# Optimization experiments

Hardware: AMD Instinct MI355X
Metric: run time of the kernel (lower is better)

The kernel has to match this reference:

```python
import jax, jax.numpy as jnp
import numpy as np

B, S, D, H = 8, 1024, 512, 8
DK = D // H
NEG = -1e30  # stands in for -inf; masked probs are zero-filled afterwards, so math matches


def setup_inputs() -> dict:
    rng = jax.random.key(0)
    ks = jax.random.split(rng, 12)
    f = lambda k, shape: jax.random.normal(k, shape, dtype=jnp.float32)
    w = lambda k: f(k, (D, D)) * 0.02  # stored as (in, out); y = x @ W + b
    return {
        "query": f(ks[0], (B, S, D)),
        "key": f(ks[1], (B, S, D)),
        "value": f(ks[2], (B, S, D)),
        "mask": jax.random.randint(ks[3], (B, 1, S), 0, 2, dtype=jnp.int32),
        "Wq": w(ks[4]), "bq": jnp.zeros((D,), jnp.float32),
        "Wk": w(ks[5]), "bk": jnp.zeros((D,), jnp.float32),
        "Wv": w(ks[6]), "bv": jnp.zeros((D,), jnp.float32),
        "Wo": w(ks[7]), "bo": jnp.zeros((D,), jnp.float32),
    }


def reference(query, key, value, mask, Wq, bq, Wk, bk, Wv, bv, Wo, bo):
    # QKV projections -> (B, H, S, DK)
    def proj(x, W, b):
        return (x @ W + b).reshape(B, -1, H, DK).transpose(0, 2, 1, 3)

    q = proj(query, Wq, bq)
    k = proj(key, Wk, bk)
    v = proj(value, Wv, bv)

    scores = jnp.einsum("bhqd,bhkd->bhqk", q, k) / jnp.sqrt(jnp.float32(DK))
    m = (mask[:, None, :, :] == 0)  # (B, 1, 1, S): True where masked out
    scores = jnp.where(m, NEG, scores)
    attn = jax.nn.softmax(scores, axis=-1)
    attn = jnp.where(m, 0.0, attn)  # dropout rate is 0.0 -> identity

    x = jnp.einsum("bhqk,bhkd->bhqd", attn, v)
    x = x.transpose(0, 2, 1, 3).reshape(B, -1, D)  # (B, S, D)
    return x @ Wo + bo
```

## Files before the change

### kernel.cpp

```cpp
#include <hip/hip_runtime.h>
#include <hip/hip_bf16.h>

#define NB 8
#define NS 1024
#define ND 512
#define NH 8
#define NDK 64

typedef __attribute__((ext_vector_type(8))) short bf16x8;
typedef __attribute__((ext_vector_type(4))) float f32x4;
typedef __attribute__((ext_vector_type(16))) float f32x16;

#define QSCALE 0.18033688011112042f
#define NEGBIG -3.0e38f

#define CVTPK(dst, a, b) \
    asm("v_cvt_pk_bf16_f32 %0, %1, %2" : "=v"(dst) : "v"(a), "v"(b))
#define PLSWAP(a, b) \
    asm("v_permlane32_swap_b32 %0, %1" : "+v"(a), "+v"(b))
#define GLOAD16(gp, lp)                                                        \
    __builtin_amdgcn_global_load_lds(                                          \
        (const __attribute__((address_space(1))) unsigned*)(gp),               \
        (__attribute__((address_space(3))) unsigned*)(lp), 16, 0, 0)

__device__ __forceinline__ unsigned short bfround(float f) {
    union { float f; unsigned u; } v; v.f = f;
    unsigned u = v.u;
    u += 0x7fffu + ((u >> 16) & 1u);
    return (unsigned short)(u >> 16);
}

__device__ __forceinline__ size_t qf_off(int s, int dk) {
    return ((size_t)(((s >> 5) * 4 + (dk >> 4)) * 64 + ((dk >> 3) & 1) * 32 + (s & 31)) << 3) + (dk & 7);
}
__device__ __forceinline__ size_t kf_off(int s, int dk) {
    return ((size_t)(((s >> 6) * 8 + ((s >> 5) & 1) * 4 + (dk >> 4)) * 64 + ((dk >> 3) & 1) * 32 + (s & 31)) << 3) + (dk & 7);
}
__device__ __forceinline__ size_t vf_off(int s, int dk) {
    return ((size_t)(((s >> 6) * 8 + (dk >> 5) * 4 + ((s >> 4) & 3)) * 64 + ((s >> 3) & 1) * 32 + (dk & 31)) << 3) + (s & 7);
}

__global__ __launch_bounds__(256) void wt_kernel(const float* __restrict__ W0,
                                                 const float* __restrict__ W1,
                                                 const float* __restrict__ W2,
                                                 const float* __restrict__ W3,
                                                 unsigned short* __restrict__ wt) {
    __shared__ float sh[64][65];
    const int z = blockIdx.z;
    const float* W = z == 0 ? W0 : z == 1 ? W1 : z == 2 ? W2 : W3;
    unsigned short* out = wt + (size_t)z * ND * ND;
    const int o0 = blockIdx.x * 64, i0 = blockIdx.y * 64;
    const int tx = threadIdx.x & 63;
    const int ty = threadIdx.x >> 6;
    #pragma unroll
    for (int rr = 0; rr < 16; ++rr) {
        const int row = ty * 16 + rr;
        sh[row][tx] = W[(size_t)(i0 + row) * ND + o0 + tx];
    }
    __syncthreads();
    #pragma unroll
    for (int rr = 0; rr < 16; ++rr) {
        const int row = ty * 16 + rr;
        out[(size_t)(o0 + row) * ND + i0 + tx] = bfround(sh[tx][row]);
    }
}

__global__ __launch_bounds__(256) void gemm_qkv(
    const float* __restrict__ A0, const float* __restrict__ A1, const float* __restrict__ A2,
    const unsigned short* __restrict__ wt,
    const float* __restrict__ b0, const float* __restrict__ b1, const float* __restrict__ b2,
    unsigned short* __restrict__ outb) {
    __shared__ float Asf[128 * 32];
    __shared__ unsigned short Bs[128 * 32];
    const int t = threadIdx.x;
    const int lane = t & 63, w = t >> 6;
    const int wr = w >> 1, wc = w & 1;
    const int lr = lane & 15, lg = lane >> 4;
    const int bid = blockIdx.x;
    const int u = (bid & 7) * 96 + (bid >> 3);
    const int xt = u & 3, yt = (u >> 2) & 63, z = u >> 8;
    const float* A = z == 0 ? A0 : z == 1 ? A1 : A2;
    const float* bias = z == 0 ? b0 : z == 1 ? b1 : b2;
    const unsigned short* Wt = wt + (size_t)z * ND * ND;
    unsigned short* outp = outb + (size_t)z * NB * NH * NS * NDK;
    const int m0 = yt * 128, n0 = xt * 128;

    const int a_row = w * 32 + (lane >> 3);
    const int a_gc = ((lane & 7) ^ (lane >> 3)) << 2;
    const int b_row = w * 32 + (lane >> 2);
    const int b_gc = (lane & 3) * 8;

    f32x4 acc[4][4];
    #pragma unroll
    for (int i = 0; i < 4; ++i)
        #pragma unroll
        for (int j = 0; j < 4; ++j) acc[i][j] = (f32x4){0.f, 0.f, 0.f, 0.f};

    for (int kt = 0; kt < 16; ++kt) {
        const int k0 = kt * 32;
        __syncthreads();
        #pragma unroll
        for (int j = 0; j < 4; ++j)
            GLOAD16(A + (size_t)(m0 + a_row + j * 8) * ND + k0 + a_gc,
                    Asf + (w * 4 + j) * 256);
        #pragma unroll
        for (int j = 0; j < 2; ++j)
            GLOAD16(Wt + (size_t)(n0 + b_row + j * 16) * ND + k0 + b_gc,
                    Bs + (w * 2 + j) * 512);
        __syncthreads();

        bf16x8 af[4], bfr[4];
        #pragma unroll
        for (int mi = 0; mi < 4; ++mi) {
            const int r = wr * 64 + mi * 16 + lr;
            const int u0 = (2 * lg) ^ (lr & 7), u1 = (2 * lg + 1) ^ (lr & 7);
            const f32x4 x0 = *(const f32x4*)(Asf + r * 32 + u0 * 4);
            const f32x4 x1 = *(const f32x4*)(Asf + r * 32 + u1 * 4);
            unsigned p0, p1, p2, p3;
            CVTPK(p0, x0[0], x0[1]); CVTPK(p1, x0[2], x0[3]);
            CVTPK(p2, x1[0], x1[1]); CVTPK(p3, x1[2], x1[3]);
            union { unsigned uu[4]; bf16x8 v; } c;
            c.uu[0] = p0; c.uu[1] = p1; c.uu[2] = p2; c.uu[3] = p3;
            af[mi] = c.v;
        }
        #pragma unroll
        for (int nj = 0; nj < 4; ++nj)
            bfr[nj] = *(const bf16x8*)(Bs + (wc * 64 + nj * 16 + lr) * 32 + lg * 8);
        #pragma unroll
        for (int mi = 0; mi < 4; ++mi)
            #pragma unroll
            for (int nj = 0; nj < 4; ++nj)
                acc[mi][nj] = __builtin_amdgcn_mfma_f32_16x16x32_bf16(
                    af[mi], bfr[nj], acc[mi][nj], 0, 0, 0);
    }

    const float osc = z == 0 ? QSCALE : 1.0f;
    #pragma unroll
    for (int mi = 0; mi < 4; ++mi) {
        #pragma unroll
        for (int nj = 0; nj < 4; ++nj) {
            const int n = n0 + wc * 64 + nj * 16 + lr;
            const float bv = bias[n];
            #pragma unroll
            for (int r = 0; r < 4; ++r) {
                const int m = m0 + wr * 64 + mi * 16 + lg * 4 + r;
                const float val = (acc[mi][nj][r] + bv) * osc;
                const int bb = m >> 10, s = m & 1023;
                const int hh = n >> 6, dk = n & 63;
                const size_t off = z == 0 ? qf_off(s, dk)
                                 : z == 1 ? kf_off(s, dk)
                                          : vf_off(s, dk);
                outp[((size_t)(bb * NH + hh) << 16) + off] = bfround(val);
            }
        }
    }
}

__global__ __launch_bounds__(256) void gemm_out(
    const unsigned short* __restrict__ Xb, const unsigned short* __restrict__ Wt,
    const float* __restrict__ bo, float* __restrict__ outp) {
    __shared__ unsigned short As[128 * 32];
    __shared__ unsigned short Bs[64 * 32];
    const int t = threadIdx.x;
    const int lane = t & 63, w = t >> 6;
    const int wr = w >> 1, wc = w & 1;
    const int lr = lane & 15, lg = lane >> 4;
    const int bid = blockIdx.x;
    const int u = (bid & 7) * 64 + (bid >> 3);
    const int xt = u & 7, yt = u >> 3;
    const int m0 = yt * 128, n0 = xt * 64;

    const int a_row = w * 32 + (lane >> 2);
    const int b_row = w * 16 + (lane >> 2);
    const int gc = (lane & 3) * 8;

    f32x4 acc[4][2];
    #pragma unroll
    for (int i = 0; i < 4; ++i)
        #pragma unroll
        for (int j = 0; j < 2; ++j) acc[i][j] = (f32x4){0.f, 0.f, 0.f, 0.f};

    for (int kt = 0; kt < 16; ++kt) {
        const int k0 = kt * 32;
        __syncthreads();
        #pragma unroll
        for (int j = 0; j < 2; ++j)
            GLOAD16(Xb + (size_t)(m0 + a_row + j * 16) * ND + k0 + gc,
                    As + (w * 2 + j) * 512);
        GLOAD16(Wt + (size_t)(n0 + b_row) * ND + k0 + gc, Bs + w * 512);
        __syncthreads();

        bf16x8 af[4], bfr[2];
        #pragma unroll
        for (int mi = 0; mi < 4; ++mi)
            af[mi] = *(const bf16x8*)(As + (wr * 64 + mi * 16 + lr) * 32 + lg * 8);
        #pragma unroll
        for (int nj = 0; nj < 2; ++nj)
            bfr[nj] = *(const bf16x8*)(Bs + (wc * 32 + nj * 16 + lr) * 32 + lg * 8);
        #pragma unroll
        for (int mi = 0; mi < 4; ++mi)
            #pragma unroll
            for (int nj = 0; nj < 2; ++nj)
                acc[mi][nj] = __builtin_amdgcn_mfma_f32_16x16x32_bf16(
                    af[mi], bfr[nj], acc[mi][nj], 0, 0, 0);
    }

    #pragma unroll
    for (int mi = 0; mi < 4; ++mi) {
        #pragma unroll
        for (int nj = 0; nj < 2; ++nj) {
            const int n = n0 + wc * 32 + nj * 16 + lr;
            const float bv = bo[n];
            #pragma unroll
            for (int r = 0; r < 4; ++r) {
                const int m = m0 + wr * 64 + mi * 16 + lg * 4 + r;
                outp[(size_t)m * ND + n] = acc[mi][nj][r] + bv;
            }
        }
    }
}

struct AttnState {
    f32x16 acc0, acc1;
    float m_st, l_st;
};

__device__ __forceinline__ void attn_step(const bf16x8 (&kf)[8], const bf16x8 (&vv)[8],
                                          const bf16x8 (&qf)[4], int mval,
                                          float* __restrict__ brow, int lane, int hi,
                                          AttnState& st) {
    brow[lane] = mval ? 0.f : NEGBIG;

    f32x16 sc0 = {}, sc1 = {};
    __builtin_amdgcn_s_setprio(1);
    sc0 = __builtin_amdgcn_mfma_f32_32x32x16_bf16(kf[0], qf[0], sc0, 0, 0, 0);
    sc1 = __builtin_amdgcn_mfma_f32_32x32x16_bf16(kf[4], qf[0], sc1, 0, 0, 0);
    sc0 = __builtin_amdgcn_mfma_f32_32x32x16_bf16(kf[1], qf[1], sc0, 0, 0, 0);
    sc1 = __builtin_amdgcn_mfma_f32_32x32x16_bf16(kf[5], qf[1], sc1, 0, 0, 0);
    sc0 = __builtin_amdgcn_mfma_f32_32x32x16_bf16(kf[2], qf[2], sc0, 0, 0, 0);
    sc1 = __builtin_amdgcn_mfma_f32_32x32x16_bf16(kf[6], qf[2], sc1, 0, 0, 0);
    sc0 = __builtin_amdgcn_mfma_f32_32x32x16_bf16(kf[3], qf[3], sc0, 0, 0, 0);
    sc1 = __builtin_amdgcn_mfma_f32_32x32x16_bf16(kf[7], qf[3], sc1, 0, 0, 0);
    __builtin_amdgcn_s_setprio(0);

    {
        const float* bl = brow + 4 * hi;
        #pragma unroll
        for (int mm = 0; mm < 4; ++mm) {
            const f32x4 bv0 = *(const f32x4*)(bl + 8 * mm);
            const f32x4 bv1 = *(const f32x4*)(bl + 32 + 8 * mm);
            #pragma unroll
            for (int c = 0; c < 4; ++c) {
                sc0[4 * mm + c] += bv0[c];
                sc1[4 * mm + c] += bv1[c];
            }
        }
    }

    float tv[16];
    #pragma unroll
    for (int r = 0; r < 16; ++r) tv[r] = fmaxf(sc0[r], sc1[r]);
    #pragma unroll
    for (int s = 8; s > 0; s >>= 1)
        #pragma unroll
        for (int r = 0; r < 16; ++r)
            if (r < s) tv[r] = fmaxf(tv[r], tv[r + s]);
    const float mx = fmaxf(tv[0], __shfl_xor(tv[0], 32));
    const float mn = fmaxf(st.m_st, mx);

    #pragma unroll
    for (int r = 0; r < 16; ++r) {
        sc0[r] = __builtin_amdgcn_exp2f(sc0[r] - mn);
        sc1[r] = __builtin_amdgcn_exp2f(sc1[r] - mn);
    }
    #pragma unroll
    for (int r = 0; r < 16; ++r) tv[r] = sc0[r] + sc1[r];
    #pragma unroll
    for (int s = 8; s > 0; s >>= 1)
        #pragma unroll
        for (int r = 0; r < 16; ++r)
            if (r < s) tv[r] += tv[r + s];
    const float rs = tv[0] + __shfl_xor(tv[0], 32);

    const bool ch = mn > st.m_st;
    if (__any(ch)) {
        const float f = __builtin_amdgcn_exp2f(st.m_st - mn);
        st.l_st = st.l_st * f + rs;
        st.m_st = mn;
        #pragma unroll
        for (int r = 0; r < 16; ++r) { st.acc0[r] *= f; st.acc1[r] *= f; }
    } else {
        st.l_st += rs;
    }

    union U8 { unsigned u[4]; bf16x8 v; };
    bf16x8 pA0, pA1, pB0, pB1;
    {
        unsigned w00, w01, w10, w11, w20, w21, w30, w31;
        CVTPK(w00, sc0[0], sc0[1]);  CVTPK(w01, sc0[2], sc0[3]);
        CVTPK(w10, sc0[4], sc0[5]);  CVTPK(w11, sc0[6], sc0[7]);
        CVTPK(w20, sc0[8], sc0[9]);  CVTPK(w21, sc0[10], sc0[11]);
        CVTPK(w30, sc0[12], sc0[13]); CVTPK(w31, sc0[14], sc0[15]);
        PLSWAP(w00, w10); PLSWAP(w01, w11);
        PLSWAP(w20, w30); PLSWAP(w21, w31);
        U8 f0; f0.u[0] = w00; f0.u[1] = w01; f0.u[2] = w10; f0.u[3] = w11;
        U8 f1; f1.u[0] = w20; f1.u[1] = w21; f1.u[2] = w30; f1.u[3] = w31;
        pA0 = f0.v; pA1 = f1.v;
    }
    {
        unsigned w00, w01, w10, w11, w20, w21, w30, w31;
        CVTPK(w00, sc1[0], sc1[1]);  CVTPK(w01, sc1[2], sc1[3]);
        CVTPK(w10, sc1[4], sc1[5]);  CVTPK(w11, sc1[6], sc1[7]);
        CVTPK(w20, sc1[8], sc1[9]);  CVTPK(w21, sc1[10], sc1[11]);
        CVTPK(w30, sc1[12], sc1[13]); CVTPK(w31, sc1[14], sc1[15]);
        PLSWAP(w00, w10); PLSWAP(w01, w11);
        PLSWAP(w20, w30); PLSWAP(w21, w31);
        U8 f0; f0.u[0] = w00; f0.u[1] = w01; f0.u[2] = w10; f0.u[3] = w11;
        U8 f1; f1.u[0] = w20; f1.u[1] = w21; f1.u[2] = w30; f1.u[3] = w31;
        pB0 = f0.v; pB1 = f1.v;
    }

    __builtin_amdgcn_s_setprio(1);
    st.acc0 = __builtin_amdgcn_mfma_f32_32x32x16_bf16(vv[0], pA0, st.acc0, 0, 0, 0);
    st.acc1 = __builtin_amdgcn_mfma_f32_32x32x16_bf16(vv[4], pA0, st.acc1, 0, 0, 0);
    st.acc0 = __builtin_amdgcn_mfma_f32_32x32x16_bf16(vv[1], pA1, st.acc0, 0, 0, 0);
    st.acc1 = __builtin_amdgcn_mfma_f32_32x32x16_bf16(vv[5], pA1, st.acc1, 0, 0, 0);
    st.acc0 = __builtin_amdgcn_mfma_f32_32x32x16_bf16(vv[2], pB0, st.acc0, 0, 0, 0);
    st.acc1 = __builtin_amdgcn_mfma_f32_32x32x16_bf16(vv[6], pB0, st.acc1, 0, 0, 0);
    st.acc0 = __builtin_amdgcn_mfma_f32_32x32x16_bf16(vv[3], pB1, st.acc0, 0, 0, 0);
    st.acc1 = __builtin_amdgcn_mfma_f32_32x32x16_bf16(vv[7], pB1, st.acc1, 0, 0, 0);
    __builtin_amdgcn_s_setprio(0);
}

__global__ __launch_bounds__(256, 2) void attn_kernel(const unsigned short* __restrict__ QF,
                                                      const unsigned short* __restrict__ KF,
                                                      const unsigned short* __restrict__ VF,
                                                      const int* __restrict__ mask,
                                                      unsigned short* __restrict__ Xb) {
    __shared__ float bias_lds[4][64];
    const int t = threadIdx.x;
    const int lane = t & 63, w = t >> 6;
    const int q32 = lane & 31, hi = lane >> 5;
    const int bid = blockIdx.x;
    const int u = (bid & 7) * 64 + (bid >> 3);
    const int bh = u >> 3, xq = u & 7;
    const int b = bh >> 3, h = bh & 7;
    const int q = xq * 128 + w * 32 + q32;
    const unsigned short* QFh = QF + ((size_t)bh << 16);
    const unsigned short* KFh = KF + ((size_t)bh << 16);
    const unsigned short* VFh = VF + ((size_t)bh << 16);
    const int* mk = mask + b * NS;
    float* brow = &bias_lds[w][0];

    bf16x8 qf[4];
    {
        const unsigned short* Qp = QFh + (size_t)(xq * 16 + w * 4) * 512 + lane * 8;
        qf[0] = *(const bf16x8*)(Qp + 0 * 512);
        qf[1] = *(const bf16x8*)(Qp + 1 * 512);
        qf[2] = *(const bf16x8*)(Qp + 2 * 512);
        qf[3] = *(const bf16x8*)(Qp + 3 * 512);
    }

    AttnState st;
    st.acc0 = (f32x16){}; st.acc1 = (f32x16){};
    st.m_st = -1.0e30f; st.l_st = 0.f;

    bf16x8 kA[8], kB[8], vv[8];

#define LOADK(dst, itx) do {                                                   \
        const unsigned short* _p = KFh + (size_t)(itx) * 4096 + lane * 8;      \
        dst[0] = *(const bf16x8*)(_p + 0 * 512);                               \
        dst[1] = *(const bf16x8*)(_p + 1 * 512);                               \
        dst[2] = *(const bf16x8*)(_p + 2 * 512);                               \
        dst[3] = *(const bf16x8*)(_p + 3 * 512);                               \
        dst[4] = *(const bf16x8*)(_p + 4 * 512);                               \
        dst[5] = *(const bf16x8*)(_p + 5 * 512);                               \
        dst[6] = *(const bf16x8*)(_p + 6 * 512);                               \
        dst[7] = *(const bf16x8*)(_p + 7 * 512);                               \
    } while (0)

#define LOADV(dst, itx) do {                                                   \
        const unsigned short* _p = VFh + (size_t)(itx) * 4096 + lane * 8;      \
        dst[0] = *(const bf16x8*)(_p + 0 * 512);                               \
        dst[1] = *(const bf16x8*)(_p + 1 * 512);                               \
        dst[2] = *(const bf16x8*)(_p + 2 * 512);                               \
        dst[3] = *(const bf16x8*)(_p + 3 * 512);                               \
        dst[4] = *(const bf16x8*)(_p + 4 * 512);                               \
        dst[5] = *(const bf16x8*)(_p + 5 * 512);                               \
        dst[6] = *(const bf16x8*)(_p + 6 * 512);                               \
        dst[7] = *(const bf16x8*)(_p + 7 * 512);                               \
    } while (0)

    LOADK(kA, 0);
    #pragma unroll 1
    for (int ii = 0; ii < 8; ++ii) {
        const int itE = ii * 2, itO = itE + 1;
        const int mE = mk[itE * 64 + lane];
        LOADV(vv, itE);
        LOADK(kB, itO);
        __builtin_amdgcn_sched_barrier(0);
        attn_step(kA, vv, qf, mE, brow, lane, hi, st);
        const int mO = mk[itO * 64 + lane];
        const int itN = itO + 1 > 15 ? 15 : itO + 1;
        LOADV(vv, itO);
        LOADK(kA, itN);
        __builtin_amdgcn_sched_barrier(0);
        attn_step(kB, vv, qf, mO, brow, lane, hi, st);
    }
#undef LOADK
#undef LOADV

    const float inv = st.l_st > 0.f ? 1.f / st.l_st : 0.f;
    unsigned short* Xp = Xb + (size_t)(b * NS + q) * ND + h * 64 + 4 * hi;
    #pragma unroll
    for (int mm = 0; mm < 4; ++mm) {
        unsigned w0, w1;
        CVTPK(w0, st.acc0[4 * mm] * inv, st.acc0[4 * mm + 1] * inv);
        CVTPK(w1, st.acc0[4 * mm + 2] * inv, st.acc0[4 * mm + 3] * inv);
        uint2 pv; pv.x = w0; pv.y = w1;
        *(uint2*)(Xp + 8 * mm) = pv;
        CVTPK(w0, st.acc1[4 * mm] * inv, st.acc1[4 * mm + 1] * inv);
        CVTPK(w1, st.acc1[4 * mm + 2] * inv, st.acc1[4 * mm + 3] * inv);
        pv.x = w0; pv.y = w1;
        *(uint2*)(Xp + 32 + 8 * mm) = pv;
    }
}

extern "C" void kernel_launch(void* const* d_in, const int* in_sizes, int n_in,
                              void* d_out, int out_size, void* d_ws, size_t ws_size,
                              hipStream_t stream) {
    const float* query = (const float*)d_in[0];
    const float* key   = (const float*)d_in[1];
    const float* value = (const float*)d_in[2];
    const int*   mask  = (const int*)d_in[3];
    const float* Wq = (const float*)d_in[4];
    const float* bq = (const float*)d_in[5];
    const float* Wk = (const float*)d_in[6];
    const float* bk = (const float*)d_in[7];
    const float* Wv = (const float*)d_in[8];
    const float* bv = (const float*)d_in[9];
    const float* Wo = (const float*)d_in[10];
    const float* bo = (const float*)d_in[11];

    const size_t HEADSZ = (size_t)NB * NH * NS * NDK;
    unsigned short* wt = (unsigned short*)d_ws;
    unsigned short* QFb = wt + (size_t)4 * ND * ND;
    unsigned short* KFb = QFb + HEADSZ;
    unsigned short* VFb = KFb + HEADSZ;
    unsigned short* Xb  = VFb + HEADSZ;

    wt_kernel<<<dim3(8, 8, 4), 256, 0, stream>>>(Wq, Wk, Wv, Wo, wt);

    gemm_qkv<<<768, 256, 0, stream>>>(query, key, value, wt, bq, bk, bv, QFb);

    attn_kernel<<<512, 256, 0, stream>>>(QFb, KFb, VFb, mask, Xb);

    gemm_out<<<512, 256, 0, stream>>>(Xb, wt + (size_t)3 * ND * ND, bo, (float*)d_out);
}
```

Before: 82.56 us.

## Double-buffer LDS tiles in QKV and output projection GEMMs

Both projection GEMMs now keep two LDS buffers and issue global-to-LDS loads for the next K tile before computing on the current one. This replaces the two __syncthreads per iteration with a single vmcnt wait plus barrier, so load latency is meant to overlap with MFMA work. MFMA sections are also wrapped in s_setprio raises and sched barriers. The cost is doubled LDS per block, which may lower occupancy.

```diff
diff --git a/kernel.cpp b/kernel.cpp
--- a/kernel.cpp
+++ b/kernel.cpp
@@ -22,6 +22,9 @@
     __builtin_amdgcn_global_load_lds(                                          \
         (const __attribute__((address_space(1))) unsigned*)(gp),               \
         (__attribute__((address_space(3))) unsigned*)(lp), 16, 0, 0)
+#define VMCNT0() asm volatile("s_waitcnt vmcnt(0)" ::: "memory")
+#define SBAR() __builtin_amdgcn_s_barrier()
+#define SCHED0() __builtin_amdgcn_sched_barrier(0)
 
 __device__ __forceinline__ unsigned short bfround(float f) {
     union { float f; unsigned u; } v; v.f = f;
@@ -70,8 +73,8 @@
     const unsigned short* __restrict__ wt,
     const float* __restrict__ b0, const float* __restrict__ b1, const float* __restrict__ b2,
     unsigned short* __restrict__ outb) {
-    __shared__ float Asf[128 * 32];
-    __shared__ unsigned short Bs[128 * 32];
+    __shared__ float Asf[2][128 * 32];
+    __shared__ unsigned short Bs[2][128 * 32];
     const int t = threadIdx.x;
     const int lane = t & 63, w = t >> 6;
     const int wr = w >> 1, wc = w & 1;
@@ -96,43 +99,66 @@
         #pragma unroll
         for (int j = 0; j < 4; ++j) acc[i][j] = (f32x4){0.f, 0.f, 0.f, 0.f};
 
-    for (int kt = 0; kt < 16; ++kt) {
-        const int k0 = kt * 32;
-        __syncthreads();
-        #pragma unroll
-        for (int j = 0; j < 4; ++j)
-            GLOAD16(A + (size_t)(m0 + a_row + j * 8) * ND + k0 + a_gc,
-                    Asf + (w * 4 + j) * 256);
-        #pragma unroll
-        for (int j = 0; j < 2; ++j)
-            GLOAD16(Wt + (size_t)(n0 + b_row + j * 16) * ND + k0 + b_gc,
-                    Bs + (w * 2 + j) * 512);
-        __syncthreads();
-
-        bf16x8 af[4], bfr[4];
-        #pragma unroll
-        for (int mi = 0; mi < 4; ++mi) {
-            const int r = wr * 64 + mi * 16 + lr;
-            const int u0 = (2 * lg) ^ (lr & 7), u1 = (2 * lg + 1) ^ (lr & 7);
-            const f32x4 x0 = *(const f32x4*)(Asf + r * 32 + u0 * 4);
-            const f32x4 x1 = *(const f32x4*)(Asf + r * 32 + u1 * 4);
-            unsigned p0, p1, p2, p3;
-            CVTPK(p0, x0[0], x0[1]); CVTPK(p1, x0[2], x0[3]);
-            CVTPK(p2, x1[0], x1[1]); CVTPK(p3, x1[2], x1[3]);
-            union { unsigned uu[4]; bf16x8 v; } c;
-            c.uu[0] = p0; c.uu[1] = p1; c.uu[2] = p2; c.uu[3] = p3;
-            af[mi] = c.v;
-        }
-        #pragma unroll
-        for (int nj = 0; nj < 4; ++nj)
-            bfr[nj] = *(const bf16x8*)(Bs + (wc * 64 + nj * 16 + lr) * 32 + lg * 8);
-        #pragma unroll
-        for (int mi = 0; mi < 4; ++mi)
-            #pragma unroll
-            for (int nj = 0; nj < 4; ++nj)
-                acc[mi][nj] = __builtin_amdgcn_mfma_f32_16x16x32_bf16(
-                    af[mi], bfr[nj], acc[mi][nj], 0, 0, 0);
-    }
+#define QKV_STAGE(p, kt) do {                                                  \
+        const int _k0 = (kt) * 32;                                             \
+        GLOAD16(A + (size_t)(m0 + a_row + 0)  * ND + _k0 + a_gc, &Asf[p][(w * 4 + 0) * 256]); \
+        GLOAD16(A + (size_t)(m0 + a_row + 8)  * ND + _k0 + a_gc, &Asf[p][(w * 4 + 1) * 256]); \
+        GLOAD16(A + (size_t)(m0 + a_row + 16) * ND + _k0 + a_gc, &Asf[p][(w * 4 + 2) * 256]); \
+        GLOAD16(A + (size_t)(m0 + a_row + 24) * ND + _k0 + a_gc, &Asf[p][(w * 4 + 3) * 256]); \
+        GLOAD16(Wt + (size_t)(n0 + b_row + 0)  * ND + _k0 + b_gc, &Bs[p][(w * 2 + 0) * 512]); \
+        GLOAD16(Wt + (size_t)(n0 + b_row + 16) * ND + _k0 + b_gc, &Bs[p][(w * 2 + 1) * 512]); \
+    } while (0)
+
+#define QKV_COMPUTE(p) do {                                                    \
+        const float* _Ab = &Asf[p][0];                                         \
+        const unsigned short* _Bb = &Bs[p][0];                                 \
+        bf16x8 af[4], bfr[4];                                                  \
+        _Pragma("unroll")                                                      \
+        for (int mi = 0; mi < 4; ++mi) {                                       \
+            const int r = wr * 64 + mi * 16 + lr;                              \
+            const int u0 = (2 * lg) ^ (lr & 7);                                \
+            const f32x4 x0 = *(const f32x4*)(_Ab + r * 32 + u0 * 4);           \
+            const f32x4 x1 = *(const f32x4*)(_Ab + r * 32 + (u0 ^ 1) * 4);     \
+            unsigned c0, c1, c2, c3;                                           \
+            CVTPK(c0, x0[0], x0[1]); CVTPK(c1, x0[2], x0[3]);                  \
+            CVTPK(c2, x1[0], x1[1]); CVTPK(c3, x1[2], x1[3]);                  \
+            union { unsigned uu[4]; bf16x8 v; } cc;                            \
+            cc.uu[0] = c0; cc.uu[1] = c1; cc.uu[2] = c2; cc.uu[3] = c3;        \
+            af[mi] = cc.v;                                                     \
+        }                                                                      \
+        _Pragma("unroll")                                                      \
+        for (int nj = 0; nj < 4; ++nj)                                         \
+            bfr[nj] = *(const bf16x8*)(_Bb + (wc * 64 + nj * 16 + lr) * 32 + lg * 8); \
+        __builtin_amdgcn_s_setprio(1);                                         \
+        _Pragma("unroll")                                                      \
+        for (int mi = 0; mi < 4; ++mi)                                         \
+            _Pragma("unroll")                                                  \
+            for (int nj = 0; nj < 4; ++nj)                                     \
+                acc[mi][nj] = __builtin_amdgcn_mfma_f32_16x16x32_bf16(         \
+                    af[mi], bfr[nj], acc[mi][nj], 0, 0, 0);                    \
+        __builtin_amdgcn_s_setprio(0);                                         \
+    } while (0)
+
+    QKV_STAGE(0, 0);
+    VMCNT0();
+    SBAR();
+    #pragma unroll 1
+    for (int ii = 0; ii < 8; ++ii) {
+        QKV_STAGE(1, 2 * ii + 1);
+        SCHED0();
+        QKV_COMPUTE(0);
+        SCHED0();
+        VMCNT0();
+        SBAR();
+        if (ii < 7) { QKV_STAGE(0, 2 * ii + 2); }
+        SCHED0();
+        QKV_COMPUTE(1);
+        SCHED0();
+        VMCNT0();
+        SBAR();
+    }
+#undef QKV_STAGE
+#undef QKV_COMPUTE
 
     const float osc = z == 0 ? QSCALE : 1.0f;
     #pragma unroll
@@ -159,8 +185,8 @@
 __global__ __launch_bounds__(256) void gemm_out(
     const unsigned short* __restrict__ Xb, const unsigned short* __restrict__ Wt,
     const float* __restrict__ bo, float* __restrict__ outp) {
-    __shared__ unsigned short As[128 * 32];
-    __shared__ unsigned short Bs[64 * 32];
+    __shared__ unsigned short As2[2][128 * 32];
+    __shared__ unsigned short Bs2[2][64 * 32];
     const int t = threadIdx.x;
     const int lane = t & 63, w = t >> 6;
     const int wr = w >> 1, wc = w & 1;
@@ -180,30 +206,53 @@
         #pragma unroll
         for (int j = 0; j < 2; ++j) acc[i][j] = (f32x4){0.f, 0.f, 0.f, 0.f};
 
-    for (int kt = 0; kt < 16; ++kt) {
-        const int k0 = kt * 32;
-        __syncthreads();
-        #pragma unroll
-        for (int j = 0; j < 2; ++j)
-            GLOAD16(Xb + (size_t)(m0 + a_row + j * 16) * ND + k0 + gc,
-                    As + (w * 2 + j) * 512);
-        GLOAD16(Wt + (size_t)(n0 + b_row) * ND + k0 + gc, Bs + w * 512);
-        __syncthreads();
-
-        bf16x8 af[4], bfr[2];
-        #pragma unroll
-        for (int mi = 0; mi < 4; ++mi)
-            af[mi] = *(const bf16x8*)(As + (wr * 64 + mi * 16 + lr) * 32 + lg * 8);
-        #pragma unroll
-        for (int nj = 0; nj < 2; ++nj)
-            bfr[nj] = *(const bf16x8*)(Bs + (wc * 32 + nj * 16 + lr) * 32 + lg * 8);
-        #pragma unroll
-        for (int mi = 0; mi < 4; ++mi)
-            #pragma unroll
-            for (int nj = 0; nj < 2; ++nj)
-                acc[mi][nj] = __builtin_amdgcn_mfma_f32_16x16x32_bf16(
-                    af[mi], bfr[nj], acc[mi][nj], 0, 0, 0);
-    }
+#define OUT_STAGE(p, kt) do {                                                  \
+        const int _k0 = (kt) * 32;                                             \
+        GLOAD16(Xb + (size_t)(m0 + a_row + 0)  * ND + _k0 + gc, &As2[p][(w * 2 + 0) * 512]); \
+        GLOAD16(Xb + (size_t)(m0 + a_row + 16) * ND + _k0 + gc, &As2[p][(w * 2 + 1) * 512]); \
+        GLOAD16(Wt + (size_t)(n0 + b_row) * ND + _k0 + gc, &Bs2[p][w * 512]);  \
+    } while (0)
+
+#define OUT_COMPUTE(p) do {                                                    \
+        const unsigned short* _Ab = &As2[p][0];                                \
+        const unsigned short* _Bb = &Bs2[p][0];                                \
+        bf16x8 af[4], bfr[2];                                                  \
+        _Pragma("unroll")                                                      \
+        for (int mi = 0; mi < 4; ++mi)                                         \
+            af[mi] = *(const bf16x8*)(_Ab + (wr * 64 + mi * 16 + lr) * 32 + lg * 8); \
+        _Pragma("unroll")                                                      \
+        for (int nj = 0; nj < 2; ++nj)                                         \
+            bfr[nj] = *(const bf16x8*)(_Bb + (wc * 32 + nj * 16 + lr) * 32 + lg * 8); \
+        __builtin_amdgcn_s_setprio(1);                                         \
+        _Pragma("unroll")                                                      \
+        for (int mi = 0; mi < 4; ++mi)                                         \
+            _Pragma("unroll")                                                  \
+            for (int nj = 0; nj < 2; ++nj)                                     \
+                acc[mi][nj] = __builtin_amdgcn_mfma_f32_16x16x32_bf16(         \
+                    af[mi], bfr[nj], acc[mi][nj], 0, 0, 0);                    \
+        __builtin_amdgcn_s_setprio(0);                                         \
+    } while (0)
+
+    OUT_STAGE(0, 0);
+    VMCNT0();
+    SBAR();
+    #pragma unroll 1
+    for (int ii = 0; ii < 8; ++ii) {
+        OUT_STAGE(1, 2 * ii + 1);
+        SCHED0();
+        OUT_COMPUTE(0);
+        SCHED0();
+        VMCNT0();
+        SBAR();
+        if (ii < 7) { OUT_STAGE(0, 2 * ii + 2); }
+        SCHED0();
+        OUT_COMPUTE(1);
+        SCHED0();
+        VMCNT0();
+        SBAR();
+    }
+#undef OUT_STAGE
+#undef OUT_COMPUTE
 
     #pragma unroll
     for (int mi = 0; mi < 4; ++mi) {
```

After: 82.83 us. No clear change (+0.3%).
